# Kernel tuning notes

Measured on AMD Instinct MI355X. Metric: run time of the kernel, lower is better.

The kernel has to match this reference:

```python
import jax, jax.numpy as jnp
import numpy as np

NUM_EXPERTS = 8
TOP_K = 2
N_EMBD = 1024
B, T = 4, 2048


def setup_inputs() -> dict:
    key = jax.random.key(0)
    k_x, k_g, k_e = jax.random.split(key, 3)
    x = jax.random.normal(k_x, (B, T, N_EMBD), dtype=jnp.float32)
    # torch nn.Linear weight layout: (out_features, in_features); y = x @ W.T
    scale = 1.0 / np.sqrt(N_EMBD)
    gate_w = jax.random.uniform(k_g, (NUM_EXPERTS, N_EMBD), dtype=jnp.float32,
                                minval=-scale, maxval=scale)
    expert_w = jax.random.uniform(k_e, (NUM_EXPERTS, N_EMBD, N_EMBD), dtype=jnp.float32,
                                  minval=-scale, maxval=scale)
    return {"x": x, "gate_w": gate_w, "expert_w": expert_w}


def reference(x, gate_w, expert_w):
    Bb, Tt, C = x.shape
    xf = x.reshape(Bb * Tt, C)                        # (N, C)
    logits = xf @ gate_w.T                            # (N, E)
    w, sel = jax.lax.top_k(logits, TOP_K)             # (N, K) each
    # softmax over the selected logits in float32, cast back (matches torch)
    w = jax.nn.softmax(w.astype(jnp.float32), axis=1).astype(xf.dtype)
    # scatter per-token routing weights into a dense (N, E) combine matrix
    n = xf.shape[0]
    w_full = jnp.zeros((n, NUM_EXPERTS), dtype=xf.dtype)
    w_full = w_full.at[jnp.arange(n)[:, None], sel].add(w)
    # all-expert outputs: y_e = x @ W_e.T  -> (N, E, C)
    expert_out = jnp.einsum('nc,edc->ned', xf, expert_w)
    out = jnp.einsum('ne,ned->nd', w_full, expert_out)  # combine
    return out.reshape(Bb, Tt, C)
```

## Files before the change

kernel.cpp:

```cpp
#include <hip/hip_runtime.h>
#include <hip/hip_bf16.h>

#define NEXP 8
#define NEMB 1024
#define NTOK 8192
#define BM 256
#define BN 256
#define BK 64
#define NK  (NEMB / BK)
#define NIT (NK / 2)
#define BLD_STRIPE 512

typedef __attribute__((ext_vector_type(8))) short  bf16x8;
typedef __attribute__((ext_vector_type(8))) unsigned short u16x8;
typedef __attribute__((ext_vector_type(4))) float  f32x4;

#define XB_BYTES   (NTOK * NEMB * 2)
#define WB_BYTES   (NEXP * NEMB * NEMB * 2)
#define CNT_OFF    (XB_BYTES + WB_BYTES)
#define LTOK_OFF   (CNT_OFF + 256)
#define LWT_OFF    (LTOK_OFF + NEXP * NTOK * 4)
#define SELW_OFF   (LWT_OFF + NEXP * NTOK * 4)

__device__ __forceinline__ unsigned short f2bf(float f) {
    unsigned u = __builtin_bit_cast(unsigned, f);
    unsigned r = (u + 0x7fffu + ((u >> 16) & 1u)) >> 16;
    return (unsigned short)r;
}

__global__ void k_cvt_w(const float* __restrict__ w, unsigned short* __restrict__ wb) {
    int i = (blockIdx.x * blockDim.x + threadIdx.x) * 8;
    f32x4 v0 = *reinterpret_cast<const f32x4*>(w + i);
    f32x4 v1 = *reinterpret_cast<const f32x4*>(w + i + 4);
    u16x8 o;
#pragma unroll
    for (int j = 0; j < 4; ++j) { o[j] = f2bf(v0[j]); o[4 + j] = f2bf(v1[j]); }
    *reinterpret_cast<u16x8*>(wb + i) = o;
}

__global__ __launch_bounds__(256)
void k_gate(const float* __restrict__ x, const float* __restrict__ gw,
            unsigned short* __restrict__ xb, int4* __restrict__ selw) {
    int t = threadIdx.x, wave = t >> 6, lane = t & 63;
    int n = blockIdx.x * 4 + wave;

    const float* xr = x + (size_t)n * NEMB + lane * 16;
    f32x4 xv[4];
#pragma unroll
    for (int j = 0; j < 4; ++j) xv[j] = *reinterpret_cast<const f32x4*>(xr + j * 4);

    u16x8 o0, o1;
#pragma unroll
    for (int q = 0; q < 4; ++q) {
        o0[q] = f2bf(xv[0][q]); o0[4 + q] = f2bf(xv[1][q]);
        o1[q] = f2bf(xv[2][q]); o1[4 + q] = f2bf(xv[3][q]);
    }
    u16x8* xo = reinterpret_cast<u16x8*>(xb + (size_t)n * NEMB + lane * 16);
    xo[0] = o0; xo[1] = o1;

    float p[NEXP];
#pragma unroll
    for (int e = 0; e < NEXP; ++e) {
        const float* gr = gw + e * NEMB + lane * 16;
        f32x4 a = xv[0] * *reinterpret_cast<const f32x4*>(gr);
#pragma unroll
        for (int j = 1; j < 4; ++j) a += xv[j] * *reinterpret_cast<const f32x4*>(gr + j * 4);
        p[e] = a[0] + a[1] + a[2] + a[3];
    }
#pragma unroll
    for (int e = 0; e < NEXP; ++e) {
        float v = p[e];
#pragma unroll
        for (int m = 1; m < 64; m <<= 1) v += __shfl_xor(v, m, 64);
        p[e] = v;
    }
    if (lane == 0) {
        int e0 = 0; float b0 = p[0];
#pragma unroll
        for (int e = 1; e < NEXP; ++e) if (p[e] > b0) { b0 = p[e]; e0 = e; }
        int e1 = -1; float b1 = -3.4e38f;
#pragma unroll
        for (int e = 0; e < NEXP; ++e) if (e != e0 && p[e] > b1) { b1 = p[e]; e1 = e; }
        float ex = __expf(b1 - b0);
        float inv = 1.f / (1.f + ex);
        int4 s;
        s.x = e0; s.y = e1;
        s.z = __float_as_int(inv); s.w = __float_as_int(ex * inv);
        selw[n] = s;
    }
}

__global__ __launch_bounds__(256)
void k_build(const int4* __restrict__ selw, int* __restrict__ counts,
             int* __restrict__ ltok, float* __restrict__ lwt) {
    int e = blockIdx.y;
    int n0 = blockIdx.x * BLD_STRIPE;
    __shared__ int lcnt, base;
    __shared__ int   toks[BLD_STRIPE];
    __shared__ float wts[BLD_STRIPE];
    if (threadIdx.x == 0) lcnt = 0;
    __syncthreads();
    for (int i = threadIdx.x; i < BLD_STRIPE; i += 256) {
        int4 s = selw[n0 + i];
        if (s.x == e) {
            int p = atomicAdd(&lcnt, 1);
            toks[p] = n0 + i; wts[p] = __int_as_float(s.z);
        }
        if (s.y == e) {
            int p = atomicAdd(&lcnt, 1);
            toks[p] = n0 + i; wts[p] = __int_as_float(s.w);
        }
    }
    __syncthreads();
    if (threadIdx.x == 0) base = atomicAdd(&counts[e], lcnt);
    __syncthreads();
    for (int i = threadIdx.x; i < lcnt; i += 256) {
        ltok[e * NTOK + base + i] = toks[i];
        lwt[e * NTOK + base + i]  = wts[i];
    }
}

__global__ void k_pad(const int* __restrict__ counts, int* __restrict__ ltok,
                      float* __restrict__ lwt) {
    int e = blockIdx.x;
    int c = counts[e];
    int cp = (c + BM - 1) & ~(BM - 1);
    for (int i = c + threadIdx.x; i < cp; i += blockDim.x) {
        ltok[e * NTOK + i] = -1;
        lwt[e * NTOK + i]  = 0.f;
    }
}

__global__ __launch_bounds__(512, 2)
void k_gemm(const unsigned short* __restrict__ xb, const unsigned short* __restrict__ wb,
            const int* __restrict__ counts, const int* __restrict__ ltok,
            const float* __restrict__ lwt, float* __restrict__ out) {
    int e  = blockIdx.z;
    int rb = blockIdx.y;
    int cb = blockIdx.x;
    if (rb * BM >= counts[e]) return;

    __shared__ unsigned short As[2][BM * BK];
    __shared__ unsigned short Bs[2][BN * BK];
    __shared__ int   tokS[BM];
    __shared__ float wS[BM];

    int t = threadIdx.x, lane = t & 63, wave = t >> 6;
    int wr = wave >> 2, wc = wave & 3;
    int fr = lane & 15, fq = lane >> 4, fs = fr & 7;
    int pk0 = fq ^ fs, pk1 = (fq + 4) ^ fs;

    if (t < BM) {
        tokS[t] = ltok[e * NTOK + rb * BM + t];
        wS[t]   = lwt[e * NTOK + rb * BM + t];
    }

    int c0 = t & 7, r0 = t >> 3;
    int csw = c0 ^ (r0 & 7);
    const unsigned short* aS[4];
    const unsigned short* bS[4];
#pragma unroll
    for (int j = 0; j < 4; ++j) {
        int row = j * 64 + r0;
        int tok = ltok[e * NTOK + rb * BM + row];
        int tokc = tok < 0 ? 0 : tok;
        aS[j] = xb + (size_t)tokc * NEMB + csw * 8;
        bS[j] = wb + (size_t)e * NEMB * NEMB + (size_t)(cb * BN + row) * NEMB + csw * 8;
    }
    int off0 = wave * 512;
    int off1 = 4096 + wave * 512;

#define GLL(src, dst)                                                                \
    __builtin_amdgcn_global_load_lds(                                                \
        (const __attribute__((address_space(1))) void*)(src),                        \
        (__attribute__((address_space(3))) void*)(dst), 16, 0, 0)
#define STG_A(buf, h, kt) if ((kt) < NK) {                                           \
    GLL(aS[(h)*2 + 0] + (kt)*BK, &As[buf][(h)*8192 + off0]);                         \
    GLL(aS[(h)*2 + 1] + (kt)*BK, &As[buf][(h)*8192 + off1]); }
#define STG_B(buf, h, kt) if ((kt) < NK) {                                           \
    GLL(bS[(h)*2 + 0] + (kt)*BK, &Bs[buf][(h)*8192 + off0]);                         \
    GLL(bS[(h)*2 + 1] + (kt)*BK, &Bs[buf][(h)*8192 + off1]); }

#define LDA(mh, buf) { _Pragma("unroll")                                             \
    for (int m = 0; m < 4; ++m) {                                                    \
        int row = ((mh)*4 + m)*32 + wr*16 + fr;                                      \
        af[m][0] = *reinterpret_cast<const bf16x8*>(&As[buf][row*BK + pk0*8]);       \
        af[m][1] = *reinterpret_cast<const bf16x8*>(&As[buf][row*BK + pk1*8]); } }
#define LDB(dst, nh, buf) { _Pragma("unroll")                                        \
    for (int n = 0; n < 2; ++n) {                                                    \
        int row = ((nh)*2 + n)*64 + wc*16 + fr;                                      \
        dst[n][0] = *reinterpret_cast<const bf16x8*>(&Bs[buf][row*BK + pk0*8]);      \
        dst[n][1] = *reinterpret_cast<const bf16x8*>(&Bs[buf][row*BK + pk1*8]); } }
#define MM(mh, nh, bfx) { _Pragma("unroll")                                          \
    for (int m = 0; m < 4; ++m) { _Pragma("unroll")                                  \
        for (int n = 0; n < 2; ++n) {                                                \
            acc[(mh)*4+m][(nh)*2+n] = __builtin_amdgcn_mfma_f32_16x16x32_bf16(       \
                af[m][0], bfx[n][0], acc[(mh)*4+m][(nh)*2+n], 0, 0, 0);              \
            acc[(mh)*4+m][(nh)*2+n] = __builtin_amdgcn_mfma_f32_16x16x32_bf16(       \
                af[m][1], bfx[n][1], acc[(mh)*4+m][(nh)*2+n], 0, 0, 0); } } }
#define BAR   __builtin_amdgcn_s_barrier()
#define LGKM0 asm volatile("s_waitcnt lgkmcnt(0)" ::: "memory")
#define VM6   asm volatile("s_waitcnt vmcnt(6)" ::: "memory")
#define VM0   asm volatile("s_waitcnt vmcnt(0)" ::: "memory")
#define PRI1  __builtin_amdgcn_s_setprio(1)
#define PRI0  __builtin_amdgcn_s_setprio(0)

    f32x4 acc[8][4];
#pragma unroll
    for (int m = 0; m < 8; ++m)
#pragma unroll
        for (int n = 0; n < 4; ++n) acc[m][n] = (f32x4){0.f, 0.f, 0.f, 0.f};

    bf16x8 af[4][2], bf0[2][2], bf1[2][2];

    STG_A(0, 0, 0); STG_B(0, 0, 0); STG_A(0, 1, 0); STG_B(0, 1, 0);
    STG_A(1, 0, 1); STG_B(1, 0, 1); STG_B(1, 1, 1);
    VM6; LGKM0; BAR;

    for (int i = 0; i < NIT; ++i) {
        int kt1 = 2 * i + 1;
        int n0  = 2 * i + 2;
        int n1  = 2 * i + 3;
        bool lastIt = (i == NIT - 1);

        LDA(0, 0); LDB(bf0, 0, 0);
        STG_A(1, 1, kt1);
        BAR; LGKM0; PRI1; MM(0, 0, bf0); PRI0; BAR;
        LDB(bf1, 1, 0);
        STG_A(0, 0, n0);
        BAR; LGKM0; PRI1; MM(0, 1, bf1); PRI0; BAR;
        LDA(1, 0);
        STG_B(0, 0, n0);
        BAR; LGKM0; PRI1; MM(1, 0, bf0); PRI0; BAR;
        STG_A(0, 1, n0);
        if (lastIt) { VM0; } else { VM6; }
        BAR; PRI1; MM(1, 1, bf1); PRI0; BAR;
        LDA(0, 1); LDB(bf0, 0, 1);
        STG_B(0, 1, n0);
        BAR; LGKM0; PRI1; MM(0, 0, bf0); PRI0; BAR;
        LDB(bf1, 1, 1);
        STG_A(1, 0, n1);
        BAR; LGKM0; PRI1; MM(0, 1, bf1); PRI0; BAR;
        LDA(1, 1);
        STG_B(1, 0, n1);
        BAR; LGKM0; PRI1; MM(1, 0, bf0); PRI0; BAR;
        STG_B(1, 1, n1);
        if (!lastIt) { VM6; }
        BAR; PRI1; MM(1, 1, bf1); PRI0; BAR;
    }

#undef GLL
#undef STG_A
#undef STG_B
#undef LDA
#undef LDB
#undef MM

#pragma unroll
    for (int m = 0; m < 8; ++m) {
#pragma unroll
        for (int jj = 0; jj < 4; ++jj) {
            int row = m * 32 + wr * 16 + fq * 4 + jj;
            int tok = tokS[row];
            if (tok < 0) continue;
            float wgt = wS[row];
            float* orow = out + (size_t)tok * NEMB + cb * BN + wc * 16 + fr;
#pragma unroll
            for (int n = 0; n < 4; ++n)
                unsafeAtomicAdd(orow + n * 64, wgt * acc[m][n][jj]);
        }
    }
}

extern "C" void kernel_launch(void* const* d_in, const int* in_sizes, int n_in,
                              void* d_out, int out_size, void* d_ws, size_t ws_size,
                              hipStream_t stream) {
    const float* x  = (const float*)d_in[0];
    const float* gw = (const float*)d_in[1];
    const float* ew = (const float*)d_in[2];
    float* out = (float*)d_out;

    char* ws = (char*)d_ws;
    unsigned short* xb = (unsigned short*)(ws);
    unsigned short* wb = (unsigned short*)(ws + XB_BYTES);
    int*   counts = (int*)(ws + CNT_OFF);
    int*   ltok   = (int*)(ws + LTOK_OFF);
    float* lwt    = (float*)(ws + LWT_OFF);
    int4*  selw   = (int4*)(ws + SELW_OFF);

    hipMemsetAsync(counts, 0, 8 * sizeof(int), stream);
    hipMemsetAsync(out, 0, (size_t)NTOK * NEMB * sizeof(float), stream);

    k_cvt_w<<<4096, 256, 0, stream>>>(ew, wb);
    k_gate<<<NTOK / 4, 256, 0, stream>>>(x, gw, xb, selw);
    k_build<<<dim3(NTOK / BLD_STRIPE, NEXP), 256, 0, stream>>>(selw, counts, ltok, lwt);
    k_pad<<<8, 128, 0, stream>>>(counts, ltok, lwt);
    k_gemm<<<dim3(NEMB / BN, 16, NEXP), 512, 0, stream>>>(xb, wb, counts, ltok, lwt, out);
}
```

Baseline: 146.4 us.

## Split-K expert GEMM over compact tile worklist and fuse prep kernels

Merges the weight conversion and gating kernels into one launch. A padding kernel now also builds a compact list of active work tiles, where each tile is (expert, row block, column block, K half). The GEMM launches a fixed grid, with blocks remapped so consecutive tiles land across XCDs, and each block processes half of K. The aim is to remove empty blocks, improve load balance and occupancy across CUs, and cut launch overhead. In exchange, every output element gets two partial contributions, presumably accumulated atomically into the zeroed output, which adds atomic traffic.

After: 182.3 us. 24.5% more time.

```diff
diff --git a/kernel.cpp b/kernel.cpp
--- a/kernel.cpp
+++ b/kernel.cpp
@@ -8,7 +8,7 @@
 #define BN 256
 #define BK 64
 #define NK  (NEMB / BK)
-#define NIT (NK / 2)
+#define MAXT 640
 #define BLD_STRIPE 512
 
 typedef __attribute__((ext_vector_type(8))) short  bf16x8;
@@ -21,6 +21,7 @@
 #define LTOK_OFF   (CNT_OFF + 256)
 #define LWT_OFF    (LTOK_OFF + NEXP * NTOK * 4)
 #define SELW_OFF   (LWT_OFF + NEXP * NTOK * 4)
+#define META_OFF   (SELW_OFF + NTOK * 16)
 
 __device__ __forceinline__ unsigned short f2bf(float f) {
     unsigned u = __builtin_bit_cast(unsigned, f);
@@ -28,21 +29,22 @@
     return (unsigned short)r;
 }
 
-__global__ void k_cvt_w(const float* __restrict__ w, unsigned short* __restrict__ wb) {
-    int i = (blockIdx.x * blockDim.x + threadIdx.x) * 8;
-    f32x4 v0 = *reinterpret_cast<const f32x4*>(w + i);
-    f32x4 v1 = *reinterpret_cast<const f32x4*>(w + i + 4);
-    u16x8 o;
-#pragma unroll
-    for (int j = 0; j < 4; ++j) { o[j] = f2bf(v0[j]); o[4 + j] = f2bf(v1[j]); }
-    *reinterpret_cast<u16x8*>(wb + i) = o;
-}
-
 __global__ __launch_bounds__(256)
-void k_gate(const float* __restrict__ x, const float* __restrict__ gw,
+void k_prep(const float* __restrict__ x, const float* __restrict__ gw,
+            const float* __restrict__ ew, unsigned short* __restrict__ wb,
             unsigned short* __restrict__ xb, int4* __restrict__ selw) {
+    if (blockIdx.x < 4096) {
+        int i = (blockIdx.x * 256 + threadIdx.x) * 8;
+        f32x4 v0 = *reinterpret_cast<const f32x4*>(ew + i);
+        f32x4 v1 = *reinterpret_cast<const f32x4*>(ew + i + 4);
+        u16x8 o;
+#pragma unroll
+        for (int j = 0; j < 4; ++j) { o[j] = f2bf(v0[j]); o[4 + j] = f2bf(v1[j]); }
+        *reinterpret_cast<u16x8*>(wb + i) = o;
+        return;
+    }
     int t = threadIdx.x, wave = t >> 6, lane = t & 63;
-    int n = blockIdx.x * 4 + wave;
+    int n = (blockIdx.x - 4096) * 4 + wave;
 
     const float* xr = x + (size_t)n * NEMB + lane * 16;
     f32x4 xv[4];
@@ -120,25 +122,46 @@
     }
 }
 
-__global__ void k_pad(const int* __restrict__ counts, int* __restrict__ ltok,
-                      float* __restrict__ lwt) {
-    int e = blockIdx.x;
-    int c = counts[e];
-    int cp = (c + BM - 1) & ~(BM - 1);
-    for (int i = c + threadIdx.x; i < cp; i += blockDim.x) {
-        ltok[e * NTOK + i] = -1;
-        lwt[e * NTOK + i]  = 0.f;
+__global__ void k_padW(const int* __restrict__ counts, int* __restrict__ ltok,
+                       float* __restrict__ lwt, int* __restrict__ meta) {
+    __shared__ int nt[NEXP], off[NEXP];
+    int t = threadIdx.x;
+    if (t < NEXP) nt[t] = (counts[t] + BM - 1) / BM;
+    __syncthreads();
+    if (t == 0) {
+        int T = 0;
+        for (int e = 0; e < NEXP; ++e) { off[e] = T; T += nt[e] * 8; }
+        meta[0] = T;
+    }
+    __syncthreads();
+    for (int e = 0; e < NEXP; ++e) {
+        int ne = nt[e] * 8;
+        for (int j = t; j < ne; j += 256) {
+            int rb = j >> 3, q = j & 7, cb = q >> 1, kh = q & 1;
+            meta[16 + off[e] + j] = (e << 16) | (rb << 8) | (cb << 4) | kh;
+        }
+        int c = counts[e], cp = nt[e] * BM;
+        for (int i = c + t; i < cp; i += 256) {
+            ltok[e * NTOK + i] = -1;
+            lwt[e * NTOK + i]  = 0.f;
+        }
     }
 }
 
 __global__ __launch_bounds__(512, 2)
 void k_gemm(const unsigned short* __restrict__ xb, const unsigned short* __restrict__ wb,
-            const int* __restrict__ counts, const int* __restrict__ ltok,
-            const float* __restrict__ lwt, float* __restrict__ out) {
-    int e  = blockIdx.z;
-    int rb = blockIdx.y;
-    int cb = blockIdx.x;
-    if (rb * BM >= counts[e]) return;
+            const int* __restrict__ ltok, const float* __restrict__ lwt,
+            const int* __restrict__ meta, float* __restrict__ out) {
+    int T = meta[0];
+    int slot = (blockIdx.x & 7) * (MAXT / 8) + (blockIdx.x >> 3);
+    if (slot >= T) return;
+    int wle = meta[16 + slot];
+    int e  = wle >> 16;
+    int rb = (wle >> 8) & 255;
+    int cb = (wle >> 4) & 15;
+    int kh = wle & 15;
+    int kB = kh * (NK / 2);
+    int kE = kB + NK / 2;
 
     __shared__ unsigned short As[2][BM * BK];
     __shared__ unsigned short Bs[2][BN * BK];
@@ -174,10 +197,10 @@
     __builtin_amdgcn_global_load_lds(                                                \
         (const __attribute__((address_space(1))) void*)(src),                        \
         (__attribute__((address_space(3))) void*)(dst), 16, 0, 0)
-#define STG_A(buf, h, kt) if ((kt) < NK) {                                           \
+#define STG_A(buf, h, kt) if ((kt) < kE) {                                           \
     GLL(aS[(h)*2 + 0] + (kt)*BK, &As[buf][(h)*8192 + off0]);                         \
     GLL(aS[(h)*2 + 1] + (kt)*BK, &As[buf][(h)*8192 + off1]); }
-#define STG_B(buf, h, kt) if ((kt) < NK) {                                           \
+#define STG_B(buf, h, kt) if ((kt) < kE) {                                           \
     GLL(bS[(h)*2 + 0] + (kt)*BK, &Bs[buf][(h)*8192 + off0]);                         \
     GLL(bS[(h)*2 + 1] + (kt)*BK, &Bs[buf][(h)*8192 + off1]); }
 
@@ -213,15 +236,15 @@
 
     bf16x8 af[4][2], bf0[2][2], bf1[2][2];
 
-    STG_A(0, 0, 0); STG_B(0, 0, 0); STG_A(0, 1, 0); STG_B(0, 1, 0);
-    STG_A(1, 0, 1); STG_B(1, 0, 1); STG_B(1, 1, 1);
+    STG_A(0, 0, kB); STG_B(0, 0, kB); STG_A(0, 1, kB); STG_B(0, 1, kB);
+    STG_A(1, 0, kB + 1); STG_B(1, 0, kB + 1); STG_B(1, 1, kB + 1);
     VM6; LGKM0; BAR;
 
-    for (int i = 0; i < NIT; ++i) {
-        int kt1 = 2 * i + 1;
-        int n0  = 2 * i + 2;
-        int n1  = 2 * i + 3;
-        bool lastIt = (i == NIT - 1);
+    for (int i = 0; i < 4; ++i) {
+        int kt1 = kB + 2 * i + 1;
+        int n0  = kB + 2 * i + 2;
+        int n1  = kB + 2 * i + 3;
+        bool lastIt = (i == 3);
 
         LDA(0, 0); LDB(bf0, 0, 0);
         STG_A(1, 1, kt1);
@@ -287,13 +310,13 @@
     int*   ltok   = (int*)(ws + LTOK_OFF);
     float* lwt    = (float*)(ws + LWT_OFF);
     int4*  selw   = (int4*)(ws + SELW_OFF);
+    int*   meta   = (int*)(ws + META_OFF);
 
     hipMemsetAsync(counts, 0, 8 * sizeof(int), stream);
     hipMemsetAsync(out, 0, (size_t)NTOK * NEMB * sizeof(float), stream);
 
-    k_cvt_w<<<4096, 256, 0, stream>>>(ew, wb);
-    k_gate<<<NTOK / 4, 256, 0, stream>>>(x, gw, xb, selw);
+    k_prep<<<4096 + NTOK / 4, 256, 0, stream>>>(x, gw, ew, wb, xb, selw);
     k_build<<<dim3(NTOK / BLD_STRIPE, NEXP), 256, 0, stream>>>(selw, counts, ltok, lwt);
-    k_pad<<<8, 128, 0, stream>>>(counts, ltok, lwt);
-    k_gemm<<<dim3(NEMB / BN, 16, NEXP), 512, 0, stream>>>(xb, wb, counts, ltok, lwt, out);
-}
+    k_padW<<<1, 256, 0, stream>>>(counts, ltok, lwt, meta);
+    k_gemm<<<MAXT, 512, 0, stream>>>(xb, wb, ltok, lwt, meta, out);
+}
```

## Split expert GEMM into full-tile main kernel and 128-row remainder kernel

Applied to the files above, without the earlier changes.

The grouped GEMM now runs in two kernels. A 256x256 tiled kernel covers only the full 256-row blocks of each expert, using a flattened grid with the expert index varying fastest. A smaller single-buffered 128x128 kernel covers up to two 128-row remainder blocks per expert, cutting the MFMA work spent on padded rows. The weight conversion and gating kernels are merged into one launch, and the pad kernel is replaced by a memset of the token lists to -1. The fixed main grid of 384 blocks assumes no expert receives more than 12 full tiles, so heavily skewed routing would drop rows.

New measurement: 146.2 us. No clear change (-0.2%).

```diff
diff --git a/kernel.cpp b/kernel.cpp
--- a/kernel.cpp
+++ b/kernel.cpp
@@ -4,8 +4,6 @@
 #define NEXP 8
 #define NEMB 1024
 #define NTOK 8192
-#define BM 256
-#define BN 256
 #define BK 64
 #define NK  (NEMB / BK)
 #define NIT (NK / 2)
@@ -28,21 +26,22 @@
     return (unsigned short)r;
 }
 
-__global__ void k_cvt_w(const float* __restrict__ w, unsigned short* __restrict__ wb) {
-    int i = (blockIdx.x * blockDim.x + threadIdx.x) * 8;
-    f32x4 v0 = *reinterpret_cast<const f32x4*>(w + i);
-    f32x4 v1 = *reinterpret_cast<const f32x4*>(w + i + 4);
-    u16x8 o;
-#pragma unroll
-    for (int j = 0; j < 4; ++j) { o[j] = f2bf(v0[j]); o[4 + j] = f2bf(v1[j]); }
-    *reinterpret_cast<u16x8*>(wb + i) = o;
-}
-
 __global__ __launch_bounds__(256)
-void k_gate(const float* __restrict__ x, const float* __restrict__ gw,
+void k_prep(const float* __restrict__ x, const float* __restrict__ gw,
+            const float* __restrict__ ew, unsigned short* __restrict__ wb,
             unsigned short* __restrict__ xb, int4* __restrict__ selw) {
+    if (blockIdx.x < 4096) {
+        int i = (blockIdx.x * 256 + threadIdx.x) * 8;
+        f32x4 v0 = *reinterpret_cast<const f32x4*>(ew + i);
+        f32x4 v1 = *reinterpret_cast<const f32x4*>(ew + i + 4);
+        u16x8 o;
+#pragma unroll
+        for (int j = 0; j < 4; ++j) { o[j] = f2bf(v0[j]); o[4 + j] = f2bf(v1[j]); }
+        *reinterpret_cast<u16x8*>(wb + i) = o;
+        return;
+    }
     int t = threadIdx.x, wave = t >> 6, lane = t & 63;
-    int n = blockIdx.x * 4 + wave;
+    int n = (blockIdx.x - 4096) * 4 + wave;
 
     const float* xr = x + (size_t)n * NEMB + lane * 16;
     f32x4 xv[4];
@@ -120,39 +119,29 @@
     }
 }
 
-__global__ void k_pad(const int* __restrict__ counts, int* __restrict__ ltok,
-                      float* __restrict__ lwt) {
-    int e = blockIdx.x;
-    int c = counts[e];
-    int cp = (c + BM - 1) & ~(BM - 1);
-    for (int i = c + threadIdx.x; i < cp; i += blockDim.x) {
-        ltok[e * NTOK + i] = -1;
-        lwt[e * NTOK + i]  = 0.f;
-    }
-}
-
 __global__ __launch_bounds__(512, 2)
-void k_gemm(const unsigned short* __restrict__ xb, const unsigned short* __restrict__ wb,
-            const int* __restrict__ counts, const int* __restrict__ ltok,
-            const float* __restrict__ lwt, float* __restrict__ out) {
-    int e  = blockIdx.z;
-    int rb = blockIdx.y;
-    int cb = blockIdx.x;
-    if (rb * BM >= counts[e]) return;
-
-    __shared__ unsigned short As[2][BM * BK];
-    __shared__ unsigned short Bs[2][BN * BK];
-    __shared__ int   tokS[BM];
-    __shared__ float wS[BM];
+void k_gemm_main(const unsigned short* __restrict__ xb, const unsigned short* __restrict__ wb,
+                 const int* __restrict__ counts, const int* __restrict__ ltok,
+                 const float* __restrict__ lwt, float* __restrict__ out) {
+    int e  = blockIdx.x & 7;
+    int bi = blockIdx.x >> 3;
+    int rb = bi >> 2;
+    int cb = bi & 3;
+    if (rb >= (counts[e] >> 8)) return;
+
+    __shared__ unsigned short As[2][256 * BK];
+    __shared__ unsigned short Bs[2][256 * BK];
+    __shared__ int   tokS[256];
+    __shared__ float wS[256];
 
     int t = threadIdx.x, lane = t & 63, wave = t >> 6;
     int wr = wave >> 2, wc = wave & 3;
     int fr = lane & 15, fq = lane >> 4, fs = fr & 7;
     int pk0 = fq ^ fs, pk1 = (fq + 4) ^ fs;
 
-    if (t < BM) {
-        tokS[t] = ltok[e * NTOK + rb * BM + t];
-        wS[t]   = lwt[e * NTOK + rb * BM + t];
+    if (t < 256) {
+        tokS[t] = ltok[e * NTOK + rb * 256 + t];
+        wS[t]   = lwt[e * NTOK + rb * 256 + t];
     }
 
     int c0 = t & 7, r0 = t >> 3;
@@ -162,10 +151,10 @@
 #pragma unroll
     for (int j = 0; j < 4; ++j) {
         int row = j * 64 + r0;
-        int tok = ltok[e * NTOK + rb * BM + row];
+        int tok = ltok[e * NTOK + rb * 256 + row];
         int tokc = tok < 0 ? 0 : tok;
         aS[j] = xb + (size_t)tokc * NEMB + csw * 8;
-        bS[j] = wb + (size_t)e * NEMB * NEMB + (size_t)(cb * BN + row) * NEMB + csw * 8;
+        bS[j] = wb + (size_t)e * NEMB * NEMB + (size_t)(cb * 256 + row) * NEMB + csw * 8;
     }
     int off0 = wave * 512;
     int off1 = 4096 + wave * 512;
@@ -217,33 +206,40 @@
     STG_A(1, 0, 1); STG_B(1, 0, 1); STG_B(1, 1, 1);
     VM6; LGKM0; BAR;
 
-    for (int i = 0; i < NIT; ++i) {
-        int kt1 = 2 * i + 1;
-        int n0  = 2 * i + 2;
-        int n1  = 2 * i + 3;
-        bool lastIt = (i == NIT - 1);
+    for (int it = 0; it < NIT; ++it) {
+        int kt1 = 2 * it + 1;
+        int n0  = 2 * it + 2;
+        int n1  = 2 * it + 3;
+        bool lastIt = (it == NIT - 1);
 
         LDA(0, 0); LDB(bf0, 0, 0);
         STG_A(1, 1, kt1);
         BAR; LGKM0; PRI1; MM(0, 0, bf0); PRI0; BAR;
+
         LDB(bf1, 1, 0);
         STG_A(0, 0, n0);
         BAR; LGKM0; PRI1; MM(0, 1, bf1); PRI0; BAR;
+
         LDA(1, 0);
         STG_B(0, 0, n0);
         BAR; LGKM0; PRI1; MM(1, 0, bf0); PRI0; BAR;
+
         STG_A(0, 1, n0);
         if (lastIt) { VM0; } else { VM6; }
         BAR; PRI1; MM(1, 1, bf1); PRI0; BAR;
+
         LDA(0, 1); LDB(bf0, 0, 1);
         STG_B(0, 1, n0);
         BAR; LGKM0; PRI1; MM(0, 0, bf0); PRI0; BAR;
+
         LDB(bf1, 1, 1);
         STG_A(1, 0, n1);
         BAR; LGKM0; PRI1; MM(0, 1, bf1); PRI0; BAR;
+
         LDA(1, 1);
         STG_B(1, 0, n1);
         BAR; LGKM0; PRI1; MM(1, 0, bf0); PRI0; BAR;
+
         STG_B(1, 1, n1);
         if (!lastIt) { VM6; }
         BAR; PRI1; MM(1, 1, bf1); PRI0; BAR;
@@ -255,6 +251,12 @@
 #undef LDA
 #undef LDB
 #undef MM
+#undef BAR
+#undef LGKM0
+#undef VM6
+#undef VM0
+#undef PRI1
+#undef PRI0
 
 #pragma unroll
     for (int m = 0; m < 8; ++m) {
@@ -264,10 +266,109 @@
             int tok = tokS[row];
             if (tok < 0) continue;
             float wgt = wS[row];
-            float* orow = out + (size_t)tok * NEMB + cb * BN + wc * 16 + fr;
+            float* orow = out + (size_t)tok * NEMB + cb * 256 + wc * 16 + fr;
 #pragma unroll
             for (int n = 0; n < 4; ++n)
                 unsafeAtomicAdd(orow + n * 64, wgt * acc[m][n][jj]);
+        }
+    }
+}
+
+__global__ __launch_bounds__(256)
+void k_gemm_rem(const unsigned short* __restrict__ xb, const unsigned short* __restrict__ wb,
+                const int* __restrict__ counts, const int* __restrict__ ltok,
+                const float* __restrict__ lwt, float* __restrict__ out) {
+    int e    = blockIdx.x & 7;
+    int j    = blockIdx.x >> 3;
+    int cb   = j & 7;
+    int slot = j >> 3;
+    int cnt  = counts[e];
+    int rb   = ((cnt >> 8) << 1) + slot;
+    if (rb * 128 >= cnt) return;
+
+    __shared__ unsigned short As[128 * BK];
+    __shared__ unsigned short Bs[128 * BK];
+    __shared__ int   tokS[128];
+    __shared__ float wS[128];
+
+    int t = threadIdx.x, lane = t & 63, wave = t >> 6;
+    int wr = wave >> 1, wc = wave & 1;
+    int fr = lane & 15, fq = lane >> 4, fs = fr & 7;
+
+    if (t < 128) {
+        tokS[t] = ltok[e * NTOK + rb * 128 + t];
+        wS[t]   = lwt[e * NTOK + rb * 128 + t];
+    }
+
+    const unsigned short* aSrc[4];
+    const unsigned short* bSrc[4];
+    int ldsOff[4];
+#pragma unroll
+    for (int i = 0; i < 4; ++i) {
+        int idx = i * 256 + t;
+        int r   = idx >> 3;
+        int csw = (idx & 7) ^ (r & 7);
+        int tok = ltok[e * NTOK + rb * 128 + r];
+        int tokc = tok < 0 ? 0 : tok;
+        aSrc[i] = xb + (size_t)tokc * NEMB + csw * 8;
+        bSrc[i] = wb + (size_t)e * NEMB * NEMB + (size_t)(cb * 128 + r) * NEMB + csw * 8;
+        ldsOff[i] = (i * 256 + wave * 64) * 8;
+    }
+
+    f32x4 acc[4][4];
+#pragma unroll
+    for (int m = 0; m < 4; ++m)
+#pragma unroll
+        for (int n = 0; n < 4; ++n) acc[m][n] = (f32x4){0.f, 0.f, 0.f, 0.f};
+
+    for (int kk = 0; kk < NK; ++kk) {
+#pragma unroll
+        for (int i = 0; i < 4; ++i) {
+            __builtin_amdgcn_global_load_lds(
+                (const __attribute__((address_space(1))) void*)(aSrc[i] + kk * BK),
+                (__attribute__((address_space(3))) void*)(As + ldsOff[i]), 16, 0, 0);
+            __builtin_amdgcn_global_load_lds(
+                (const __attribute__((address_space(1))) void*)(bSrc[i] + kk * BK),
+                (__attribute__((address_space(3))) void*)(Bs + ldsOff[i]), 16, 0, 0);
+        }
+        __syncthreads();
+
+#pragma unroll
+        for (int ks = 0; ks < 2; ++ks) {
+            int ch = (fq + 4 * ks) ^ fs;
+            bf16x8 af[4], bfr[4];
+#pragma unroll
+            for (int m = 0; m < 4; ++m)
+                af[m] = *reinterpret_cast<const bf16x8*>(
+                    As + (wr * 64 + m * 16 + fr) * BK + ch * 8);
+#pragma unroll
+            for (int n = 0; n < 4; ++n)
+                bfr[n] = *reinterpret_cast<const bf16x8*>(
+                    Bs + (wc * 64 + n * 16 + fr) * BK + ch * 8);
+            __builtin_amdgcn_s_setprio(1);
+#pragma unroll
+            for (int m = 0; m < 4; ++m)
+#pragma unroll
+                for (int n = 0; n < 4; ++n)
+                    acc[m][n] = __builtin_amdgcn_mfma_f32_16x16x32_bf16(
+                        af[m], bfr[n], acc[m][n], 0, 0, 0);
+            __builtin_amdgcn_s_setprio(0);
+        }
+        __syncthreads();
+    }
+
+#pragma unroll
+    for (int m = 0; m < 4; ++m) {
+#pragma unroll
+        for (int jj = 0; jj < 4; ++jj) {
+            int row = wr * 64 + m * 16 + fq * 4 + jj;
+            int tok = tokS[row];
+            if (tok < 0) continue;
+            float wgt = wS[row];
+            float* orow = out + (size_t)tok * NEMB + cb * 128 + wc * 64 + fr;
+#pragma unroll
+            for (int n = 0; n < 4; ++n)
+                unsafeAtomicAdd(orow + n * 16, wgt * acc[m][n][jj]);
         }
     }
 }
@@ -289,11 +390,11 @@
     int4*  selw   = (int4*)(ws + SELW_OFF);
 
     hipMemsetAsync(counts, 0, 8 * sizeof(int), stream);
+    hipMemsetAsync(ltok, 0xFF, NEXP * NTOK * sizeof(int), stream);
     hipMemsetAsync(out, 0, (size_t)NTOK * NEMB * sizeof(float), stream);
 
-    k_cvt_w<<<4096, 256, 0, stream>>>(ew, wb);
-    k_gate<<<NTOK / 4, 256, 0, stream>>>(x, gw, xb, selw);
+    k_prep<<<4096 + NTOK / 4, 256, 0, stream>>>(x, gw, ew, wb, xb, selw);
     k_build<<<dim3(NTOK / BLD_STRIPE, NEXP), 256, 0, stream>>>(selw, counts, ltok, lwt);
-    k_pad<<<8, 128, 0, stream>>>(counts, ltok, lwt);
-    k_gemm<<<dim3(NEMB / BN, 16, NEXP), 512, 0, stream>>>(xb, wb, counts, ltok, lwt, out);
-}
+    k_gemm_main<<<384, 512, 0, stream>>>(xb, wb, counts, ltok, lwt, out);
+    k_gemm_rem<<<8 * 8 * 2, 256, 0, stream>>>(xb, wb, counts, ltok, lwt, out);
+}
```
